# Performance work log

Measured on AMD Instinct MI355X. Metric: run time of the kernel, lower is better.

The kernel has to match this reference:

```python
import jax, jax.numpy as jnp
import numpy as np

IN_F = 512
OUT_F = 512
NOISE_DIM = 128
BATCH = 512
OUT_DIM = IN_F * OUT_F + OUT_F  # 262656
PRIOR_STD = 1.0
PRIOR_SCALE = 1.0
POSTERIOR_SCALE = 1.0


def setup_inputs() -> dict:
    key = jax.random.key(0)
    k1, k2, k3, k4, k5, k6 = jax.random.split(key, 6)
    x = jax.random.normal(k1, (BATCH, IN_F), dtype=jnp.float32)
    prior_x = jax.random.normal(k2, (BATCH, IN_F), dtype=jnp.float32)
    hyper_noise = jax.random.normal(k3, (BATCH, NOISE_DIM), dtype=jnp.float32)
    # hypermodel = nn.Linear(noise_dim, out_dim): kaiming-uniform-ish init approximated by uniform
    bound = 1.0 / np.sqrt(NOISE_DIM)
    hW = jax.random.uniform(k4, (OUT_DIM, NOISE_DIM), jnp.float32, -bound, bound)
    hb = jax.random.uniform(k5, (OUT_DIM,), jnp.float32, -bound, bound)
    # PriorHyperLinear: row-normalized gaussian weight scaled by prior_std (eye), zero bias (prior_mean=0)
    pW = jax.random.normal(k6, (OUT_DIM, NOISE_DIM), dtype=jnp.float32)
    pW = PRIOR_STD * pW / jnp.linalg.norm(pW, axis=1, keepdims=True)
    pb = jnp.zeros((OUT_DIM,), dtype=jnp.float32)
    return {"x": x, "prior_x": prior_x, "hyper_noise": hyper_noise,
            "hW": hW, "hb": hb, "pW": pW, "pb": pb}


def _base_forward(x, params):
    # params: [B, in*out + out] -> per-sample weight [B, in, out], bias [B, out]
    weight = params[:, : IN_F * OUT_F].reshape(-1, IN_F, OUT_F)
    bias = params[:, IN_F * OUT_F:]  # [B, out]
    # bmm(x[:,None,:], weight) + bias -> [B, out]
    return jnp.einsum("bi,bio->bo", x, weight) + bias


def reference(x, prior_x, hyper_noise, hW, hb, pW, pb):
    params = hyper_noise @ hW.T + hb  # [B, out_dim]
    out = _base_forward(x, params)
    prior_params = hyper_noise @ pW.T + pb
    prior_out = _base_forward(prior_x, prior_params)
    return out * POSTERIOR_SCALE + prior_out * PRIOR_SCALE
```

## Files before the change

kernel.cpp:

```cpp
#include <hip/hip_runtime.h>
#include <hip/hip_fp16.h>

#define BATCH 512
#define INF   512
#define OUTF  512
#define ND    128
#define WPART 262144
#define NSLOT 32

typedef __attribute__((ext_vector_type(8))) _Float16 half8;
typedef __attribute__((ext_vector_type(2))) _Float16 half2v;
typedef __attribute__((ext_vector_type(4))) float    f32x4;

__device__ inline half8 cvt8(float4 a, float4 b) {
  half2v h0 = __builtin_bit_cast(half2v, __builtin_amdgcn_cvt_pkrtz(a.x, a.y));
  half2v h1 = __builtin_bit_cast(half2v, __builtin_amdgcn_cvt_pkrtz(a.z, a.w));
  half2v h2 = __builtin_bit_cast(half2v, __builtin_amdgcn_cvt_pkrtz(b.x, b.y));
  half2v h3 = __builtin_bit_cast(half2v, __builtin_amdgcn_cvt_pkrtz(b.z, b.w));
  half8 r = { h0[0], h0[1], h1[0], h1[1], h2[0], h2[1], h3[0], h3[1] };
  return r;
}

__global__ void __launch_bounds__(256) tail_kernel(
    const float* __restrict__ hn, const float* __restrict__ hW,
    const float* __restrict__ pW, float* __restrict__ TT) {
  const int bt = blockIdx.x & 7;
  const int bg = blockIdx.x >> 3;
  __shared__ float wsum[64][132];
  __shared__ float hs[32][132];
  {
    int r = threadIdx.x >> 2, seg = threadIdx.x & 3;
    const float4* h4 = (const float4*)(hW + (((size_t)(WPART + bt*64 + r)) << 7) + seg*32);
    const float4* p4 = (const float4*)(pW + (((size_t)(WPART + bt*64 + r)) << 7) + seg*32);
    #pragma unroll
    for (int qq = 0; qq < 8; ++qq) {
      float4 a = h4[qq], b = p4[qq];
      float* d = &wsum[r][seg*32 + qq*4];
      d[0]=a.x+b.x; d[1]=a.y+b.y; d[2]=a.z+b.z; d[3]=a.w+b.w;
    }
    int bb = threadIdx.x >> 3, ch = threadIdx.x & 7;
    const float4* hh = (const float4*)(hn + (((size_t)(bg*32 + bb)) << 7) + ch*16);
    #pragma unroll
    for (int qq = 0; qq < 4; ++qq) {
      float4 a = hh[qq];
      float* d = &hs[bb][ch*16 + qq*4];
      d[0]=a.x; d[1]=a.y; d[2]=a.z; d[3]=a.w;
    }
  }
  __syncthreads();
  const int ol = threadIdx.x & 63, b0 = (threadIdx.x >> 6) * 8;
  float a[8] = {};
  for (int n = 0; n < 128; n += 4) {
    float4 wv = *(const float4*)&wsum[ol][n];
    #pragma unroll
    for (int r = 0; r < 8; ++r) {
      float4 hv = *(const float4*)&hs[b0 + r][n];
      a[r] += hv.x*wv.x + hv.y*wv.y + hv.z*wv.z + hv.w*wv.w;
    }
  }
  #pragma unroll
  for (int r = 0; r < 8; ++r)
    TT[(((size_t)(bg*32 + b0 + r)) << 9) + bt*64 + ol] = a[r];
}

__global__ void __launch_bounds__(512, 4) gemm_kernel(
    const float* __restrict__ x, const float* __restrict__ px,
    const float* __restrict__ hn, const float* __restrict__ hW,
    const float* __restrict__ pW, float* __restrict__ P) {
  const int tid = threadIdx.x;
  const int lane = tid & 63, w = tid >> 6;
  const int l15 = lane & 15, j = lane >> 4;
  const int wm = w >> 1, wn = w & 1;

  const int q  = blockIdx.x;
  const int nt = blockIdx.y;
  const int n0 = nt << 5;
  const int part   = q >> 4;
  const int i0     = (q & 15) << 5;
  const float* srcW = part ? pW : hW;
  const float* srcX = part ? px : x;

  __shared__ half8 ldsW[2][256];
  __shared__ unsigned short xh[512][32];

  f32x4 acc[8] = {};

  {
    const int rsub = tid >> 3, ch = tid & 7;
    const int g = ch >> 1, sub = ch & 1;
    #pragma unroll
    for (int r = 0; r < 8; ++r) {
      int row = r * 64 + rsub;
      float4 v = *(const float4*)(srcX + ((size_t)row << 9) + i0 + ch * 4);
      unsigned u0 = __builtin_bit_cast(unsigned, __builtin_amdgcn_cvt_pkrtz(v.x, v.y));
      unsigned u1 = __builtin_bit_cast(unsigned, __builtin_amdgcn_cvt_pkrtz(v.z, v.w));
      uint2 uu; uu.x = u0; uu.y = u1;
      *(uint2*)((char*)xh + row * 64 + ((g ^ (row & 3)) << 4) + sub * 8) = uu;
    }
  }

  const int o_s = tid >> 4;
  const int seg = tid & 15;
  const int isub_s = seg >> 3;
  const int nl_s   = (seg & 7) << 2;
  const int wg     = (isub_s << 2) + ((seg & 7) >> 1);
  const int wbyte  = (o_s << 7) + (((wg ^ (o_s & 7))) << 4) + ((seg & 1) << 3);

  for (int band = 0; band < 4; ++band) {
    const int woff = band << 5;

    half8 hnf[8];
    #pragma unroll
    for (int m = 0; m < 8; ++m) {
      int row = wm * 128 + m * 16 + l15;
      const float4* hp = (const float4*)(hn + ((size_t)row << 7) + woff + (j << 3));
      hnf[m] = cvt8(hp[0], hp[1]);
    }

    auto loadW = [&](int ph, float4& rw) {
      int i = i0 + 2 * ph + isub_s;
      rw = *(const float4*)(srcW +
          (((size_t)((i << 9) + n0 + o_s)) << 7) + woff + nl_s);
    };
    auto writeW = [&](int buf, float4 rw) {
      unsigned u0 = __builtin_bit_cast(unsigned, __builtin_amdgcn_cvt_pkrtz(rw.x, rw.y));
      unsigned u1 = __builtin_bit_cast(unsigned, __builtin_amdgcn_cvt_pkrtz(rw.z, rw.w));
      uint2 uu; uu.x = u0; uu.y = u1;
      *(uint2*)((char*)ldsW + buf * 4096 + wbyte) = uu;
    };
    auto compute = [&](int buf, int p) {
      const char* WB = (const char*)ldsW + buf * 4096;
      half8 bf0, bf1;
      {
        int col = wn * 16 + l15;
        int cb  = col << 7;
        bf0 = *(const half8*)(WB + cb + (((j     ) ^ (col & 7)) << 4));
        bf1 = *(const half8*)(WB + cb + (((4 + j) ^ (col & 7)) << 4));
      }
      half2v hx[8];
      #pragma unroll
      for (int m = 0; m < 8; ++m) {
        int row = wm * 128 + m * 16 + l15;
        unsigned xw = *(const unsigned*)((const char*)xh + row * 64 +
            ((((p >> 2)) ^ (row & 3)) << 4) + ((4 * p) & 15));
        hx[m] = __builtin_bit_cast(half2v, xw);
      }
      __builtin_amdgcn_s_setprio(1);
      #pragma unroll
      for (int m = 0; m < 8; ++m) {
        _Float16 lo = hx[m][0];
        half8 xb = { lo, lo, lo, lo, lo, lo, lo, lo };
        acc[m] = __builtin_amdgcn_mfma_f32_16x16x32_f16(hnf[m] * xb, bf0, acc[m], 0, 0, 0);
      }
      #pragma unroll
      for (int m = 0; m < 8; ++m) {
        _Float16 hi = hx[m][1];
        half8 xb = { hi, hi, hi, hi, hi, hi, hi, hi };
        acc[m] = __builtin_amdgcn_mfma_f32_16x16x32_f16(hnf[m] * xb, bf1, acc[m], 0, 0, 0);
      }
      __builtin_amdgcn_s_setprio(0);
    };

    float4 rwA, rwB;
    loadW(0, rwA);
    loadW(1, rwB);
    writeW(0, rwA);
    asm volatile("s_waitcnt lgkmcnt(0)" ::: "memory");
    __builtin_amdgcn_s_barrier();

    for (int p = 0; p < 14; p += 2) {
      loadW(p + 2, rwA);
      compute(0, p);
      writeW(1, rwB);
      asm volatile("s_waitcnt lgkmcnt(0)" ::: "memory");
      __builtin_amdgcn_s_barrier();

      loadW(p + 3, rwB);
      compute(1, p + 1);
      writeW(0, rwA);
      asm volatile("s_waitcnt lgkmcnt(0)" ::: "memory");
      __builtin_amdgcn_s_barrier();
    }
    compute(0, 14);
    writeW(1, rwB);
    asm volatile("s_waitcnt lgkmcnt(0)" ::: "memory");
    __builtin_amdgcn_s_barrier();
    compute(1, 15);
    __builtin_amdgcn_s_barrier();
  }

  float* outp = P + ((size_t)q << 18);
  #pragma unroll
  for (int m = 0; m < 8; ++m) {
    int row = wm * 128 + m * 16 + (j << 2);
    int col = n0 + wn * 16 + l15;
    float* op = outp + (size_t)row * OUTF + col;
    op[0]    = acc[m][0];
    op[512]  = acc[m][1];
    op[1024] = acc[m][2];
    op[1536] = acc[m][3];
  }
}

__global__ void __launch_bounds__(256) finish_kernel(
    const float* __restrict__ P, const float* __restrict__ x,
    const float* __restrict__ hb, const float* __restrict__ TT,
    float* __restrict__ out) {
  const int o  = blockIdx.x * 256 + threadIdx.x;
  const int b0 = blockIdx.y * 2;
  __shared__ float xs[2][512];
  #pragma unroll
  for (int t = 0; t < 4; ++t) {
    int idx = threadIdx.x + t * 256;
    xs[idx >> 9][idx & 511] = x[((size_t)(b0 + (idx >> 9)) << 9) + (idx & 511)];
  }
  __syncthreads();

  const float bias = hb[WPART + o];
  float a0 = bias, a1 = bias;
  #pragma unroll 16
  for (int i = 0; i < 512; ++i) {
    float hv = hb[(i << 9) + o];
    a0 += xs[0][i] * hv;
    a1 += xs[1][i] * hv;
  }
  a0 += TT[((size_t)b0 << 9) + o];
  a1 += TT[((size_t)(b0 + 1) << 9) + o];

  const float* P0 = P + ((size_t)b0 << 9) + o;
  const float* P1 = P0 + 512;
  float t00 = 0, t01 = 0, t10 = 0, t11 = 0;
  #pragma unroll 4
  for (int k = 0; k < NSLOT; k += 2) {
    t00 += P0[(size_t)(k)     << 18];
    t01 += P0[(size_t)(k + 1) << 18];
    t10 += P1[(size_t)(k)     << 18];
    t11 += P1[(size_t)(k + 1) << 18];
  }
  out[((size_t)b0 << 9) + o]       = a0 + t00 + t01;
  out[((size_t)(b0 + 1) << 9) + o] = a1 + t10 + t11;
}

extern "C" void kernel_launch(void* const* d_in, const int* in_sizes, int n_in,
                              void* d_out, int out_size, void* d_ws, size_t ws_size,
                              hipStream_t stream) {
  const float* x  = (const float*)d_in[0];
  const float* px = (const float*)d_in[1];
  const float* hn = (const float*)d_in[2];
  const float* hW = (const float*)d_in[3];
  const float* hb = (const float*)d_in[4];
  const float* pW = (const float*)d_in[5];
  float* out = (float*)d_out;
  float* TT  = (float*)d_ws;
  float* P   = TT + (1 << 18);

  tail_kernel<<<dim3(128), 256, 0, stream>>>(hn, hW, pW, TT);
  gemm_kernel<<<dim3(NSLOT, 16), dim3(512), 0, stream>>>(x, px, hn, hW, pW, P);
  finish_kernel<<<dim3(2, 256), dim3(256), 0, stream>>>(P, x, hb, TT, out);
}
```

Measured before the change: 133.6 us.

## Enlarge per-stage W tile to 8 input rows and restructure pipeline stages

The GEMM kernel now stages 8 input-feature rows by 32 noise columns of W per pipeline step instead of 2 rows, so each barrier-separated stage issues 64 MFMAs rather than 16. The band loop is flattened into 16 stages, and hyper-noise fragments are reloaded every four stages. The x tile is re-laid out so one half8 load yields eight per-row scalars. This is meant to cut barrier and LDS synchronisation overhead per MFMA and to widen global loads. In exchange it uses more LDS and registers, and the occupancy hint is dropped from the launch bounds.

```diff
diff --git a/kernel.cpp b/kernel.cpp
--- a/kernel.cpp
+++ b/kernel.cpp
@@ -63,7 +63,7 @@
     TT[(((size_t)(bg*32 + b0 + r)) << 9) + bt*64 + ol] = a[r];
 }
 
-__global__ void __launch_bounds__(512, 4) gemm_kernel(
+__global__ void __launch_bounds__(512) gemm_kernel(
     const float* __restrict__ x, const float* __restrict__ px,
     const float* __restrict__ hn, const float* __restrict__ hW,
     const float* __restrict__ pW, float* __restrict__ P) {
@@ -73,119 +73,104 @@
   const int wm = w >> 1, wn = w & 1;
 
   const int q  = blockIdx.x;
-  const int nt = blockIdx.y;
-  const int n0 = nt << 5;
-  const int part   = q >> 4;
-  const int i0     = (q & 15) << 5;
+  const int n0 = blockIdx.y << 5;
+  const int part = q >> 4;
+  const int i0   = (q & 15) << 5;
   const float* srcW = part ? pW : hW;
   const float* srcX = part ? px : x;
 
-  __shared__ half8 ldsW[2][256];
-  __shared__ unsigned short xh[512][32];
+  __shared__ half8 ldsW[2][1024];
+  __shared__ half8 xh[4][512];
 
   f32x4 acc[8] = {};
 
   {
     const int rsub = tid >> 3, ch = tid & 7;
-    const int g = ch >> 1, sub = ch & 1;
+    const int pp = ch >> 1, sub = ch & 1;
     #pragma unroll
     for (int r = 0; r < 8; ++r) {
       int row = r * 64 + rsub;
       float4 v = *(const float4*)(srcX + ((size_t)row << 9) + i0 + ch * 4);
-      unsigned u0 = __builtin_bit_cast(unsigned, __builtin_amdgcn_cvt_pkrtz(v.x, v.y));
-      unsigned u1 = __builtin_bit_cast(unsigned, __builtin_amdgcn_cvt_pkrtz(v.z, v.w));
-      uint2 uu; uu.x = u0; uu.y = u1;
-      *(uint2*)((char*)xh + row * 64 + ((g ^ (row & 3)) << 4) + sub * 8) = uu;
-    }
-  }
-
-  const int o_s = tid >> 4;
-  const int seg = tid & 15;
-  const int isub_s = seg >> 3;
-  const int nl_s   = (seg & 7) << 2;
-  const int wg     = (isub_s << 2) + ((seg & 7) >> 1);
-  const int wbyte  = (o_s << 7) + (((wg ^ (o_s & 7))) << 4) + ((seg & 1) << 3);
-
-  for (int band = 0; band < 4; ++band) {
-    const int woff = band << 5;
-
-    half8 hnf[8];
+      unsigned ua = __builtin_bit_cast(unsigned, __builtin_amdgcn_cvt_pkrtz(v.x, v.y));
+      unsigned ub = __builtin_bit_cast(unsigned, __builtin_amdgcn_cvt_pkrtz(v.z, v.w));
+      uint2 uu; uu.x = ua; uu.y = ub;
+      *(uint2*)((char*)xh + pp * 8192 + row * 16 + sub * 8) = uu;
+    }
+  }
+
+  const int il_s = tid >> 6;
+  const int o_s  = (tid >> 1) & 31;
+  const int hf_s = tid & 1;
+
+  auto loadW = [&](int g, float4* rw) {
+    int i = i0 + ((g & 3) << 3) + il_s;
+    const float4* p4 = (const float4*)(srcW +
+        (((size_t)((i << 9) + n0 + o_s)) << 7) + ((g >> 2) << 5) + (hf_s << 4));
+    rw[0] = p4[0]; rw[1] = p4[1]; rw[2] = p4[2]; rw[3] = p4[3];
+  };
+  auto writeW = [&](int buf, const float4* rw) {
+    char* base = (char*)ldsW + buf * 16384 + il_s * 2048 + hf_s * 1024 + o_s * 16;
+    *(half8*)base         = cvt8(rw[0], rw[1]);
+    *(half8*)(base + 512) = cvt8(rw[2], rw[3]);
+  };
+
+  half8 hnf[8];
+  auto loadHnf = [&](int band) {
     #pragma unroll
     for (int m = 0; m < 8; ++m) {
       int row = wm * 128 + m * 16 + l15;
-      const float4* hp = (const float4*)(hn + ((size_t)row << 7) + woff + (j << 3));
+      const float4* hp = (const float4*)(hn + ((size_t)row << 7) + (band << 5) + (j << 3));
       hnf[m] = cvt8(hp[0], hp[1]);
     }
-
-    auto loadW = [&](int ph, float4& rw) {
-      int i = i0 + 2 * ph + isub_s;
-      rw = *(const float4*)(srcW +
-          (((size_t)((i << 9) + n0 + o_s)) << 7) + woff + nl_s);
-    };
-    auto writeW = [&](int buf, float4 rw) {
-      unsigned u0 = __builtin_bit_cast(unsigned, __builtin_amdgcn_cvt_pkrtz(rw.x, rw.y));
-      unsigned u1 = __builtin_bit_cast(unsigned, __builtin_amdgcn_cvt_pkrtz(rw.z, rw.w));
-      uint2 uu; uu.x = u0; uu.y = u1;
-      *(uint2*)((char*)ldsW + buf * 4096 + wbyte) = uu;
-    };
-    auto compute = [&](int buf, int p) {
-      const char* WB = (const char*)ldsW + buf * 4096;
-      half8 bf0, bf1;
-      {
-        int col = wn * 16 + l15;
-        int cb  = col << 7;
-        bf0 = *(const half8*)(WB + cb + (((j     ) ^ (col & 7)) << 4));
-        bf1 = *(const half8*)(WB + cb + (((4 + j) ^ (col & 7)) << 4));
-      }
-      half2v hx[8];
+  };
+
+  auto compute = [&](int buf, int g) {
+    const char* WB = (const char*)ldsW + buf * 16384;
+    const int pp = g & 3;
+    half8 bfv[8], hx[8];
+    #pragma unroll
+    for (int il = 0; il < 8; ++il)
+      bfv[il] = *(const half8*)(WB + il * 2048 + j * 512 + ((wn << 4) + l15) * 16);
+    #pragma unroll
+    for (int m = 0; m < 8; ++m) {
+      int row = wm * 128 + m * 16 + l15;
+      hx[m] = *(const half8*)((const char*)xh + pp * 8192 + row * 16);
+    }
+    __builtin_amdgcn_s_setprio(1);
+    #pragma unroll
+    for (int il = 0; il < 8; ++il) {
       #pragma unroll
       for (int m = 0; m < 8; ++m) {
-        int row = wm * 128 + m * 16 + l15;
-        unsigned xw = *(const unsigned*)((const char*)xh + row * 64 +
-            ((((p >> 2)) ^ (row & 3)) << 4) + ((4 * p) & 15));
-        hx[m] = __builtin_bit_cast(half2v, xw);
+        _Float16 xs = hx[m][il];
+        half8 xb = { xs, xs, xs, xs, xs, xs, xs, xs };
+        acc[m] = __builtin_amdgcn_mfma_f32_16x16x32_f16(
+            hnf[m] * xb, bfv[il], acc[m], 0, 0, 0);
       }
-      __builtin_amdgcn_s_setprio(1);
-      #pragma unroll
-      for (int m = 0; m < 8; ++m) {
-        _Float16 lo = hx[m][0];
-        half8 xb = { lo, lo, lo, lo, lo, lo, lo, lo };
-        acc[m] = __builtin_amdgcn_mfma_f32_16x16x32_f16(hnf[m] * xb, bf0, acc[m], 0, 0, 0);
-      }
-      #pragma unroll
-      for (int m = 0; m < 8; ++m) {
-        _Float16 hi = hx[m][1];
-        half8 xb = { hi, hi, hi, hi, hi, hi, hi, hi };
-        acc[m] = __builtin_amdgcn_mfma_f32_16x16x32_f16(hnf[m] * xb, bf1, acc[m], 0, 0, 0);
-      }
-      __builtin_amdgcn_s_setprio(0);
-    };
-
-    float4 rwA, rwB;
-    loadW(0, rwA);
-    loadW(1, rwB);
-    writeW(0, rwA);
-    asm volatile("s_waitcnt lgkmcnt(0)" ::: "memory");
-    __builtin_amdgcn_s_barrier();
-
-    for (int p = 0; p < 14; p += 2) {
-      loadW(p + 2, rwA);
-      compute(0, p);
-      writeW(1, rwB);
-      asm volatile("s_waitcnt lgkmcnt(0)" ::: "memory");
-      __builtin_amdgcn_s_barrier();
-
-      loadW(p + 3, rwB);
-      compute(1, p + 1);
-      writeW(0, rwA);
-      asm volatile("s_waitcnt lgkmcnt(0)" ::: "memory");
-      __builtin_amdgcn_s_barrier();
-    }
-    compute(0, 14);
+    }
+    __builtin_amdgcn_s_setprio(0);
+  };
+
+  float4 rwA[4], rwB[4];
+  loadHnf(0);
+  loadW(0, rwA);
+  loadW(1, rwB);
+  writeW(0, rwA);
+  asm volatile("s_waitcnt lgkmcnt(0)" ::: "memory");
+  __builtin_amdgcn_s_barrier();
+
+  #pragma unroll 1
+  for (int g = 0; g < 16; g += 2) {
+    if (g > 0 && (g & 3) == 0) loadHnf(g >> 2);
+    if (g + 2 < 16) loadW(g + 2, rwA);
+    compute(0, g);
     writeW(1, rwB);
     asm volatile("s_waitcnt lgkmcnt(0)" ::: "memory");
     __builtin_amdgcn_s_barrier();
-    compute(1, 15);
+
+    if (g + 3 < 16) loadW(g + 3, rwB);
+    compute(1, g + 1);
+    if (g + 2 < 16) writeW(0, rwA);
+    asm volatile("s_waitcnt lgkmcnt(0)" ::: "memory");
     __builtin_amdgcn_s_barrier();
   }
 
@@ -193,7 +178,7 @@
   #pragma unroll
   for (int m = 0; m < 8; ++m) {
     int row = wm * 128 + m * 16 + (j << 2);
-    int col = n0 + wn * 16 + l15;
+    int col = n0 + (wn << 4) + l15;
     float* op = outp + (size_t)row * OUTF + col;
     op[0]    = acc[m][0];
     op[512]  = acc[m][1];
```

Measured after the change: 145.9 us. 1.09x slower.
